# Kernel tuning notes

Measured on AMD Instinct MI355X. Metric: run time of the kernel, lower is better.

Reference implementation:

```python
import jax, jax.numpy as jnp
import numpy as np

INPUT_SIZE = 21
HIDDEN = 50
OUTPUT = 24
BATCH = 4096
SEQ = 336


def setup_inputs() -> dict:
    key = jax.random.key(0)
    ks = jax.random.split(key, 7)
    s_ih = 1.0 / np.sqrt(HIDDEN)
    x = jax.random.normal(ks[0], (BATCH, SEQ, INPUT_SIZE), dtype=jnp.float32)
    # PyTorch LSTM params: gate order i, f, g, o stacked along dim0
    W_ih = jax.random.uniform(ks[1], (4 * HIDDEN, INPUT_SIZE), minval=-s_ih, maxval=s_ih, dtype=jnp.float32)
    W_hh = jax.random.uniform(ks[2], (4 * HIDDEN, HIDDEN), minval=-s_ih, maxval=s_ih, dtype=jnp.float32)
    b_ih = jax.random.uniform(ks[3], (4 * HIDDEN,), minval=-s_ih, maxval=s_ih, dtype=jnp.float32)
    b_hh = jax.random.uniform(ks[4], (4 * HIDDEN,), minval=-s_ih, maxval=s_ih, dtype=jnp.float32)
    s_fc = 1.0 / np.sqrt(HIDDEN)
    W_fc = jax.random.uniform(ks[5], (OUTPUT, HIDDEN), minval=-s_fc, maxval=s_fc, dtype=jnp.float32)
    b_fc = jax.random.uniform(ks[6], (OUTPUT,), minval=-s_fc, maxval=s_fc, dtype=jnp.float32)
    return {"x": x, "W_ih": W_ih, "W_hh": W_hh, "b_ih": b_ih, "b_hh": b_hh, "W_fc": W_fc, "b_fc": b_fc}


def _lstm_last(x, W_ih, W_hh, b_ih, b_hh):
    B = x.shape[0]
    H = W_hh.shape[1]
    # Precompute input projections for all timesteps: [T, B, 4H]
    x_proj = jnp.einsum('bti,gi->tbg', x, W_ih) + (b_ih + b_hh)

    def step(carry, xp):
        h, c = carry
        gates = xp + h @ W_hh.T  # [B, 4H]
        i_g, f_g, g_g, o_g = jnp.split(gates, 4, axis=-1)
        i_g = jax.nn.sigmoid(i_g)
        f_g = jax.nn.sigmoid(f_g)
        g_g = jnp.tanh(g_g)
        o_g = jax.nn.sigmoid(o_g)
        c = f_g * c + i_g * g_g
        h = o_g * jnp.tanh(c)
        return (h, c), None

    h0 = jnp.zeros((B, H), dtype=x.dtype)
    c0 = jnp.zeros((B, H), dtype=x.dtype)
    (h_last, _), _ = jax.lax.scan(step, (h0, c0), x_proj)
    return h_last


def reference(x, W_ih, W_hh, b_ih, b_hh, W_fc, b_fc):
    h_last = _lstm_last(x, W_ih, W_hh, b_ih, b_hh)  # [B, H]
    return h_last @ W_fc.T + b_fc  # [B, OUTPUT]
```

## Files before the change

### kernel.cpp

```cpp
#include <hip/hip_runtime.h>


#define T_SEQ 336
#define I_IN  21
#define HID   50
#define O_OUT 24
#define MB    16
#define NT    512
#define TPW   2
#define CH    8
#define NCH   42
#define XELEM (CH * MB * I_IN)
#define NLD   6
#define XBUFH (CH * 4 * 16 * 8)

#define HIDX(buf, kb, n, j) ((((buf)*8 + (kb))*16 + (n))*8 + (j))
#define XIDX(s, kb, n, j)   ((((s)*4 + (kb))*16 + (n))*8 + (j))

#define K_LOG2E 1.44269504088896340736f

typedef _Float16 f16x8 __attribute__((ext_vector_type(8)));
typedef float    f32x4 __attribute__((ext_vector_type(4)));

#define MFMA16(A, B, C) __builtin_amdgcn_mfma_f32_16x16x32_f16((A), (B), (C), 0, 0, 0)

static __device__ __forceinline__ float frcp(float v) { return __builtin_amdgcn_rcpf(v); }
static __device__ __forceinline__ float ex2(float v)  { return __builtin_amdgcn_exp2f(v); }
static __device__ __forceinline__ float sigm2(float g) { return frcp(1.f + ex2(g)); }
static __device__ __forceinline__ float tanh2(float g) {
    return __builtin_fmaf(-2.f, frcp(1.f + ex2(g)), 1.f);
}

__global__ __launch_bounds__(NT)
void lstm_mfma10(const float* __restrict__ x,
                 const float* __restrict__ W_ih,
                 const float* __restrict__ W_hh,
                 const float* __restrict__ b_ih,
                 const float* __restrict__ b_hh,
                 const float* __restrict__ W_fc,
                 const float* __restrict__ b_fc,
                 float* __restrict__ out)
{
    __shared__ _Float16 hbuf[2 * 8 * 16 * 8];
    __shared__ _Float16 xC[2 * XBUFH];

    const int tid  = threadIdx.x;
    const int lane = tid & 63;
    const int wv   = tid >> 6;
    const int nl   = lane & 15;
    const int q    = lane >> 4;
    const int b0   = blockIdx.x * MB;

    for (int i = tid; i < 2 * 8 * 16 * 8; i += NT) hbuf[i] = (_Float16)0.f;
    for (int i = tid; i < 2 * XBUFH;      i += NT) xC[i]   = (_Float16)0.f;

    const float* px[NLD];
    int  xdst[NLD];
    bool xv[NLD];
    float sv[NLD];
    #pragma unroll
    for (int k = 0; k < NLD; ++k) {
        const int e  = tid + k * NT;
        const int i  = e % I_IN;
        const int r  = e / I_IN;
        const int b  = r & 15;
        const int sIr = r >> 4;
        const int sI = (sIr < CH) ? sIr : 0;
        xv[k]   = (e < XELEM);
        px[k]   = x + ((size_t)(b0 + b) * T_SEQ + sI) * I_IN + i;
        xdst[k] = XIDX(sI, i >> 3, b, i & 7);
        sv[k]   = px[k][0];
    }

    f16x8 Wh[TPW][2], Wl[TPW][2];
    f16x8 Xh[TPW],    Xl[TPW];
    f32x4 biasv[TPW];
    #pragma unroll
    for (int tt = 0; tt < TPW; ++tt) {
        const int t    = wv * TPW + tt;
        const int p    = t * 16 + nl;
        const int unit = p >> 2, gate = p & 3;
        const bool vr  = (unit < HID);
        const float ws = (gate == 2) ? (2.f * K_LOG2E) : (-K_LOG2E);
        const int orig = gate * HID + unit;
        const int ub   = t * 4 + q;
        #pragma unroll
        for (int r = 0; r < 4; ++r) {
            const float bs = (r == 2) ? (2.f * K_LOG2E) : (-K_LOG2E);
            biasv[tt][r] = (ub < HID) ? (b_ih[r * HID + ub] + b_hh[r * HID + ub]) * bs : 0.f;
        }
        #pragma unroll
        for (int kc = 0; kc < 2; ++kc) {
            #pragma unroll
            for (int j = 0; j < 8; ++j) {
                const int k = kc * 32 + q * 8 + j;
                const float w = (vr && k < HID) ? W_hh[orig * HID + k] * ws : 0.f;
                const _Float16 hi = (_Float16)w;
                Wh[tt][kc][j] = hi;
                Wl[tt][kc][j] = (_Float16)(w - (float)hi);
            }
        }
        #pragma unroll
        for (int j = 0; j < 8; ++j) {
            const int k = q * 8 + j;
            const float w = (vr && k < I_IN) ? W_ih[orig * I_IN + k] * ws : 0.f;
            const _Float16 hi = (_Float16)w;
            Xh[tt][j] = hi;
            Xl[tt][j] = (_Float16)(w - (float)hi);
        }
    }

    __syncthreads();

    #pragma unroll
    for (int k = 0; k < NLD; ++k) {
        if (xv[k]) xC[xdst[k]] = (_Float16)sv[k];
        px[k] += CH * I_IN;
    }
    __syncthreads();

    const int u0 = (wv * TPW + 0) * 4 + q;
    const int u1 = (wv * TPW + 1) * 4 + q;
    const int hwo0 = ((u0 >> 3) * 16 + nl) * 8 + (u0 & 7);
    const int hwo1 = ((u1 >> 3) * 16 + nl) * 8 + (u1 & 7);
    float cst0 = 0.f, cst1 = 0.f;

    const _Float16* hb0 = &hbuf[HIDX(0, q, nl, 0)];
    const int bfo = ((q * 16) + nl) * 8;

    f32x4 xp[TPW][CH];
    #pragma unroll
    for (int s = 0; s < CH; ++s) {
        const f16x8 XN = *(const f16x8*)&xC[s * 512 + bfo];
        xp[0][s] = MFMA16(Xh[0], XN, biasv[0]);
        xp[0][s] = MFMA16(Xl[0], XN, xp[0][s]);
        xp[1][s] = MFMA16(Xh[1], XN, biasv[1]);
        xp[1][s] = MFMA16(Xl[1], XN, xp[1][s]);
    }

    for (int c = 0; c < NCH; ++c) {
        const int  rb    = (c & 1) * XBUFH;
        const int  wb    = ((c + 1) & 1) * XBUFH;
        const bool dostg = (c + 1) < NCH;
        #pragma unroll
        for (int s = 0; s < CH; ++s) {
            __syncthreads();

            if (s == 0 && dostg) {
                #pragma unroll
                for (int k = 0; k < NLD; ++k) sv[k] = px[k][0];
            }

            const int cur = s & 1, nxt = cur ^ 1;

            const _Float16* hb = hb0 + cur * 1024;
            const f16x8 B0 = *(const f16x8*)(hb);
            const f16x8 B1 = *(const f16x8*)(hb + 512);

            f32x4 a0 = xp[0][s];
            f32x4 a1 = xp[1][s];
            a0 = MFMA16(Wh[0][0], B0, a0);
            a1 = MFMA16(Wh[1][0], B0, a1);
            a0 = MFMA16(Wh[0][1], B1, a0);
            a1 = MFMA16(Wh[1][1], B1, a1);
            a0 = MFMA16(Wl[0][0], B0, a0);
            a1 = MFMA16(Wl[1][0], B0, a1);
            a0 = MFMA16(Wl[0][1], B1, a0);
            a1 = MFMA16(Wl[1][1], B1, a1);

            if (dostg && s >= 1) {
                const int sp = s - 1;
                const f16x8 XN = *(const f16x8*)&xC[wb + sp * 512 + bfo];
                xp[0][sp] = MFMA16(Xh[0], XN, biasv[0]);
                xp[0][sp] = MFMA16(Xl[0], XN, xp[0][sp]);
                xp[1][sp] = MFMA16(Xh[1], XN, biasv[1]);
                xp[1][sp] = MFMA16(Xl[1], XN, xp[1][sp]);
            }
            if (dostg && s == CH - 1) {
                const int sp = CH - 1;
                const f16x8 XN = *(const f16x8*)&xC[wb + sp * 512 + bfo];
                xp[0][sp] = MFMA16(Xh[0], XN, biasv[0]);
                xp[0][sp] = MFMA16(Xl[0], XN, xp[0][sp]);
                xp[1][sp] = MFMA16(Xh[1], XN, biasv[1]);
                xp[1][sp] = MFMA16(Xl[1], XN, xp[1][sp]);
            }

            {
                const float cc = __builtin_fmaf(sigm2(a0[1]), cst0,
                                                sigm2(a0[0]) * tanh2(a0[2]));
                cst0 = cc;
                const float h = sigm2(a0[3]) * tanh2(2.f * K_LOG2E * cc);
                hbuf[nxt * 1024 + hwo0] = (_Float16)h;
            }
            {
                const float cc = __builtin_fmaf(sigm2(a1[1]), cst1,
                                                sigm2(a1[0]) * tanh2(a1[2]));
                cst1 = cc;
                const float h = sigm2(a1[3]) * tanh2(2.f * K_LOG2E * cc);
                hbuf[nxt * 1024 + hwo1] = (_Float16)h;
            }

            if (s == 0 && dostg) {
                #pragma unroll
                for (int k = 0; k < NLD; ++k) {
                    if (xv[k]) xC[wb + xdst[k]] = (_Float16)sv[k];
                    px[k] += CH * I_IN;
                }
            }
        }
    }

    __syncthreads();
    if (tid < MB * O_OUT) {
        const int b = tid / O_OUT, o = tid % O_OUT;
        float a = b_fc[o];
        for (int u = 0; u < HID; ++u) {
            const float hv = (float)hbuf[HIDX(0, u >> 3, b, u & 7)];
            a = __builtin_fmaf(hv, W_fc[o * HID + u], a);
        }
        out[(size_t)(b0 + b) * O_OUT + o] = a;
    }
}

extern "C" void kernel_launch(void* const* d_in, const int* in_sizes, int n_in,
                              void* d_out, int out_size, void* d_ws, size_t ws_size,
                              hipStream_t stream)
{
    const float* x    = (const float*)d_in[0];
    const float* W_ih = (const float*)d_in[1];
    const float* W_hh = (const float*)d_in[2];
    const float* b_ih = (const float*)d_in[3];
    const float* b_hh = (const float*)d_in[4];
    const float* W_fc = (const float*)d_in[5];
    const float* b_fc = (const float*)d_in[6];
    float* out = (float*)d_out;

    lstm_mfma10<<<dim3(4096 / MB), dim3(NT), 0, stream>>>(
        x, W_ih, W_hh, b_ih, b_hh, W_fc, b_fc, out);
}
```

Before: 333.1 us.

## Stagger input-projection MFMAs across waves and raise recurrent MFMA priority

Waves are split into two phases. One half issues the next chunk's input-projection MFMAs before the recurrent matmul, the other half issues them after the gate nonlinearities. The aim is to stop MFMA and transcendental work from contending across waves on the same SIMD. The recurrent MFMAs are wrapped in s_setprio so the critical-path work is issued first. The cell state is kept pre-scaled by 2*log2e so one multiply drops out of the tanh(c) path; this changes the stored state's scaling and the rounding slightly.

```diff
diff --git a/kernel.cpp b/kernel.cpp
--- a/kernel.cpp
+++ b/kernel.cpp
@@ -18,6 +18,7 @@
 #define XIDX(s, kb, n, j)   ((((s)*4 + (kb))*16 + (n))*8 + (j))
 
 #define K_LOG2E 1.44269504088896340736f
+#define C2SCALE (2.f * K_LOG2E)
 
 typedef _Float16 f16x8 __attribute__((ext_vector_type(8)));
 typedef float    f32x4 __attribute__((ext_vector_type(4)));
@@ -30,9 +31,21 @@
 static __device__ __forceinline__ float tanh2(float g) {
     return __builtin_fmaf(-2.f, frcp(1.f + ex2(g)), 1.f);
 }
+static __device__ __forceinline__ float tanh2s(float g) {
+    return __builtin_fmaf(-2.f * C2SCALE, frcp(1.f + ex2(g)), C2SCALE);
+}
+
+#define XPROJ(sp)                                                        \
+    do {                                                                 \
+        const f16x8 XN = *(const f16x8*)&xC[wb + (sp) * 512 + bfo];      \
+        xp[0][(sp)] = MFMA16(Xh[0], XN, biasv[0]);                       \
+        xp[0][(sp)] = MFMA16(Xl[0], XN, xp[0][(sp)]);                    \
+        xp[1][(sp)] = MFMA16(Xh[1], XN, biasv[1]);                       \
+        xp[1][(sp)] = MFMA16(Xl[1], XN, xp[1][(sp)]);                    \
+    } while (0)
 
 __global__ __launch_bounds__(NT)
-void lstm_mfma10(const float* __restrict__ x,
+void lstm_mfma11(const float* __restrict__ x,
                  const float* __restrict__ W_ih,
                  const float* __restrict__ W_hh,
                  const float* __restrict__ b_ih,
@@ -50,6 +63,7 @@
     const int nl   = lane & 15;
     const int q    = lane >> 4;
     const int b0   = blockIdx.x * MB;
+    const int ph   = (wv ^ (wv >> 2)) & 1;
 
     for (int i = tid; i < 2 * 8 * 16 * 8; i += NT) hbuf[i] = (_Float16)0.f;
     for (int i = tid; i < 2 * XBUFH;      i += NT) xC[i]   = (_Float16)0.f;
@@ -81,12 +95,12 @@
         const int p    = t * 16 + nl;
         const int unit = p >> 2, gate = p & 3;
         const bool vr  = (unit < HID);
-        const float ws = (gate == 2) ? (2.f * K_LOG2E) : (-K_LOG2E);
+        const float ws = (gate == 2) ? C2SCALE : (-K_LOG2E);
         const int orig = gate * HID + unit;
         const int ub   = t * 4 + q;
         #pragma unroll
         for (int r = 0; r < 4; ++r) {
-            const float bs = (r == 2) ? (2.f * K_LOG2E) : (-K_LOG2E);
+            const float bs = (r == 2) ? C2SCALE : (-K_LOG2E);
             biasv[tt][r] = (ub < HID) ? (b_ih[r * HID + ub] + b_hh[r * HID + ub]) * bs : 0.f;
         }
         #pragma unroll
@@ -129,13 +143,10 @@
     const int bfo = ((q * 16) + nl) * 8;
 
     f32x4 xp[TPW][CH];
-    #pragma unroll
-    for (int s = 0; s < CH; ++s) {
-        const f16x8 XN = *(const f16x8*)&xC[s * 512 + bfo];
-        xp[0][s] = MFMA16(Xh[0], XN, biasv[0]);
-        xp[0][s] = MFMA16(Xl[0], XN, xp[0][s]);
-        xp[1][s] = MFMA16(Xh[1], XN, biasv[1]);
-        xp[1][s] = MFMA16(Xl[1], XN, xp[1][s]);
+    {
+        const int wb = 0;
+        #pragma unroll
+        for (int s = 0; s < CH; ++s) XPROJ(s);
     }
 
     for (int c = 0; c < NCH; ++c) {
@@ -157,6 +168,12 @@
             const f16x8 B0 = *(const f16x8*)(hb);
             const f16x8 B1 = *(const f16x8*)(hb + 512);
 
+            if (ph) {
+                if (dostg && s >= 1) XPROJ(s - 1);
+                if (dostg && s == CH - 1) XPROJ(CH - 1);
+            }
+
+            __builtin_amdgcn_s_setprio(1);
             f32x4 a0 = xp[0][s];
             f32x4 a1 = xp[1][s];
             a0 = MFMA16(Wh[0][0], B0, a0);
@@ -167,37 +184,28 @@
             a1 = MFMA16(Wl[1][0], B0, a1);
             a0 = MFMA16(Wl[0][1], B1, a0);
             a1 = MFMA16(Wl[1][1], B1, a1);
-
-            if (dostg && s >= 1) {
-                const int sp = s - 1;
-                const f16x8 XN = *(const f16x8*)&xC[wb + sp * 512 + bfo];
-                xp[0][sp] = MFMA16(Xh[0], XN, biasv[0]);
-                xp[0][sp] = MFMA16(Xl[0], XN, xp[0][sp]);
-                xp[1][sp] = MFMA16(Xh[1], XN, biasv[1]);
-                xp[1][sp] = MFMA16(Xl[1], XN, xp[1][sp]);
-            }
-            if (dostg && s == CH - 1) {
-                const int sp = CH - 1;
-                const f16x8 XN = *(const f16x8*)&xC[wb + sp * 512 + bfo];
-                xp[0][sp] = MFMA16(Xh[0], XN, biasv[0]);
-                xp[0][sp] = MFMA16(Xl[0], XN, xp[0][sp]);
-                xp[1][sp] = MFMA16(Xh[1], XN, biasv[1]);
-                xp[1][sp] = MFMA16(Xl[1], XN, xp[1][sp]);
-            }
+            __builtin_amdgcn_s_setprio(0);
 
             {
-                const float cc = __builtin_fmaf(sigm2(a0[1]), cst0,
-                                                sigm2(a0[0]) * tanh2(a0[2]));
+                const float tg2 = tanh2s(a0[2]);
+                const float cc  = __builtin_fmaf(sigm2(a0[1]), cst0,
+                                                 sigm2(a0[0]) * tg2);
                 cst0 = cc;
-                const float h = sigm2(a0[3]) * tanh2(2.f * K_LOG2E * cc);
+                const float h = sigm2(a0[3]) * tanh2(cc);
                 hbuf[nxt * 1024 + hwo0] = (_Float16)h;
             }
             {
-                const float cc = __builtin_fmaf(sigm2(a1[1]), cst1,
-                                                sigm2(a1[0]) * tanh2(a1[2]));
+                const float tg2 = tanh2s(a1[2]);
+                const float cc  = __builtin_fmaf(sigm2(a1[1]), cst1,
+                                                 sigm2(a1[0]) * tg2);
                 cst1 = cc;
-                const float h = sigm2(a1[3]) * tanh2(2.f * K_LOG2E * cc);
+                const float h = sigm2(a1[3]) * tanh2(cc);
                 hbuf[nxt * 1024 + hwo1] = (_Float16)h;
+            }
+
+            if (!ph) {
+                if (dostg && s >= 1) XPROJ(s - 1);
+                if (dostg && s == CH - 1) XPROJ(CH - 1);
             }
 
             if (s == 0 && dostg) {
@@ -235,6 +243,6 @@
     const float* b_fc = (const float*)d_in[6];
     float* out = (float*)d_out;
 
-    lstm_mfma10<<<dim3(4096 / MB), dim3(NT), 0, stream>>>(
+    lstm_mfma11<<<dim3(4096 / MB), dim3(NT), 0, stream>>>(
         x, W_ih, W_hh, b_ih, b_hh, W_fc, b_fc, out);
 }
```

Result: faster. 318.9 us (-4.3%).
